# Optimization experiments

Hardware: AMD Instinct MI355X
Metric: run time of the kernel (lower is better)

The kernel has to match this reference:

```python
import jax, jax.numpy as jnp
import numpy as np

B, A, T, D, H, NB, OUT = 64, 128, 6, 256, 512, 5, 401
ALPHA = 0.5
BETA = 0.5


def _lin_init(key, n_in, n_out, extra=()):
    bound = 1.0 / np.sqrt(n_in)
    kw, kb = jax.random.split(key)
    W = jax.random.uniform(kw, extra + (n_in, n_out), minval=-bound, maxval=bound, dtype=jnp.float32)
    b = jax.random.uniform(kb, extra + (n_out,), minval=-bound, maxval=bound, dtype=jnp.float32)
    return W, b


def setup_inputs() -> dict:
    key = jax.random.key(0)
    ks = jax.random.split(key, 8)
    stdv = 1.0 / np.sqrt(D)
    anchor = jax.random.uniform(ks[0], (1, 1, T, D), minval=-stdv, maxval=stdv, dtype=jnp.float32)
    sW1, sb1 = _lin_init(ks[1], D, D, (NB,))
    sW2, sb2 = _lin_init(ks[2], D, D, (NB,))
    cW1, cb1 = _lin_init(ks[3], D, D, (NB,))
    cW2, cb2 = _lin_init(ks[4], D, D, (NB,))
    dW1, db1 = _lin_init(ks[5], D, H)
    dW2, db2 = _lin_init(ks[6], H, OUT)
    final_embedding = jax.random.normal(ks[7], (B, A, D), dtype=jnp.float32)
    return {"final_embedding": final_embedding, "anchor": anchor,
            "sW1": sW1, "sb1": sb1, "sW2": sW2, "sb2": sb2,
            "cW1": cW1, "cb1": cb1, "cW2": cW2, "cb2": cb2,
            "dW1": dW1, "db1": db1, "dW2": dW2, "db2": db2}


def _mlp2(x, W1, b1, W2, b2):
    # 2-layer MLP (Linear -> ReLU -> Linear), applied to last dim
    return jax.nn.relu(x @ W1 + b1) @ W2 + b2


def reference(final_embedding, anchor, sW1, sb1, sW2, sb2, cW1, cb1, cW2, cb2, dW1, db1, dW2, db2):
    b, a = final_embedding.shape[:2]
    # s: [B, A, T, D] repeated anchors; c: [B, A, 1, D] context
    s = jnp.broadcast_to(anchor, (b, a, T, D))
    c = final_embedding[:, :, None, :]
    for i in range(NB):
        s_new = _mlp2(s, sW1[i], sb1[i], sW2[i], sb2[i])
        c_new = _mlp2(c, cW1[i], cb1[i], cW2[i], cb2[i])
        s_new = s_new * c_new                      # gate, broadcasts over T
        agg_c = jnp.max(s_new, axis=-2, keepdims=True)
        s = ALPHA * s + BETA * s_new               # sliding running mean
        c = ALPHA * c + BETA * agg_c
    # decoder MLP on trajectory embeddings s: [B, A, T, D]
    res = jax.nn.relu(s @ dW1 + db1) @ dW2 + db2   # [B, A, T, 401]
    coordinates = res[..., :160].reshape(b, a, T, 80, 2)
    av = res[..., 160:240].reshape(b, a, T, 80, 1)
    bv = res[..., 240:320].reshape(b, a, T, 80, 1)
    cv = res[..., 320:400].reshape(b, a, T, 80, 1)
    probas = res[..., -1]                          # [B, A, T]
    cov = jnp.concatenate([jnp.exp(av) * jnp.cosh(bv), jnp.sinh(bv),
                           jnp.sinh(bv), jnp.exp(-av) * jnp.cosh(bv)], axis=-1) * jnp.exp(cv)
    covariance_matrices = cov.reshape(b, a, T, 80, 2, 2)
    return (probas, coordinates, covariance_matrices)
```

## Files before the change

kernel.cpp:

```cpp
#include <hip/hip_runtime.h>
#include <math.h>


constexpr int Tn  = 6;
constexpr int Dn  = 256;
constexpr int Hn  = 512;
constexpr int NBn = 5;
constexpr int OUTn = 401;
constexpr int BA  = 8192;
constexpr int MR  = 49152;
constexpr float kAlpha = 0.5f;
constexpr float kBeta  = 0.5f;

typedef __bf16 bf16_8 __attribute__((ext_vector_type(8)));
typedef float  f32x4  __attribute__((ext_vector_type(4)));

__device__ __forceinline__ void async_copy16(const __bf16* g, __bf16* l) {
  __builtin_amdgcn_global_load_lds(
      (const __attribute__((address_space(1))) void*)g,
      (__attribute__((address_space(3))) void*)l, 16, 0, 0);
}

template<bool RELU, bool OUT_BF16>
__global__ __launch_bounds__(256) void gemm_mfma(
    const __bf16* __restrict__ A, const __bf16* __restrict__ BT,
    const float* __restrict__ bias, void* __restrict__ Cout,
    int M, int N, int K)
{
  __shared__ __align__(16) char smem[34816];

  const int tid = threadIdx.x;
  const int l   = tid & 63;
  const int w   = tid >> 6;
  const int wm  = w >> 1, wn = w & 1;

  const int GX = gridDim.x;
  const int total = GX * gridDim.y;
  const int L = blockIdx.y * GX + blockIdx.x;
  const int xcd = L & 7, pos = L >> 3;
  const int base = total >> 3, rem = total & 7;
  const int start = xcd * base + (xcd < rem ? xcd : rem);
  const int TL = start + pos;
  const int my = TL / GX;
  const int nx = TL - my * GX;
  const int m0 = my * 128;
  const int n0 = nx * 128;

  const int lrow = l >> 2;
  const int lk   = (l & 3) * 8;
  int ar0 = m0 + w * 32 + lrow;        if (ar0 > M - 1) ar0 = M - 1;
  int ar1 = m0 + w * 32 + 16 + lrow;   if (ar1 > M - 1) ar1 = M - 1;
  int br0 = n0 + w * 32 + lrow;        if (br0 > N - 1) br0 = N - 1;
  int br1 = n0 + w * 32 + 16 + lrow;   if (br1 > N - 1) br1 = N - 1;
  const __bf16* Ag0 = A  + (size_t)ar0 * K + lk;
  const __bf16* Ag1 = A  + (size_t)ar1 * K + lk;
  const __bf16* Bg0 = BT + (size_t)br0 * K + lk;
  const __bf16* Bg1 = BT + (size_t)br1 * K + lk;

  f32x4 acc[4][4];
#pragma unroll
  for (int i = 0; i < 4; ++i)
#pragma unroll
    for (int j = 0; j < 4; ++j) acc[i][j] = (f32x4){0.f, 0.f, 0.f, 0.f};

  auto stage = [&](int buf, int ko) {
    __bf16* As = (__bf16*)(smem + buf * 16384);
    __bf16* Bs = As + 4096;
    async_copy16(Ag0 + ko, As + w * 1024);
    async_copy16(Ag1 + ko, As + w * 1024 + 512);
    async_copy16(Bg0 + ko, Bs + w * 1024);
    async_copy16(Bg1 + ko, Bs + w * 1024 + 512);
  };

  const int kIters = K >> 5;
  stage(0, 0);
  __syncthreads();
  for (int kt = 0; kt < kIters; ++kt) {
    if (kt + 1 < kIters) stage((kt + 1) & 1, (kt + 1) * 32);
    const __bf16* As = (const __bf16*)(smem + (kt & 1) * 16384);
    const __bf16* Bs = As + 4096;
    const __bf16* ap = As + (wm * 64 + (l & 15)) * 32 + (l >> 4) * 8;
    const __bf16* bp = Bs + (wn * 64 + (l & 15)) * 32 + (l >> 4) * 8;

    bf16_8 af[4], bf[4];
#pragma unroll
    for (int i = 0; i < 4; ++i) af[i] = *(const bf16_8*)(ap + i * 16 * 32);
#pragma unroll
    for (int j = 0; j < 4; ++j) bf[j] = *(const bf16_8*)(bp + j * 16 * 32);
#pragma unroll
    for (int i = 0; i < 4; ++i)
#pragma unroll
      for (int j = 0; j < 4; ++j)
        acc[i][j] = __builtin_amdgcn_mfma_f32_16x16x32_bf16(af[i], bf[j], acc[i][j], 0, 0, 0);
    __syncthreads();
  }

  const int colb = n0 + wn * 64 + (l & 15);
  const int rowb = m0 + wm * 64 + (l >> 4) * 4;

  if (OUT_BF16) {
    __bf16* Cs = (__bf16*)smem;
    const int lrb = wm * 64 + (l >> 4) * 4;
    const int lcb = wn * 64 + (l & 15);
#pragma unroll
    for (int j = 0; j < 4; ++j) {
      const float bj = bias[colb + j * 16];
#pragma unroll
      for (int i = 0; i < 4; ++i) {
#pragma unroll
        for (int r = 0; r < 4; ++r) {
          float v = acc[i][j][r] + bj;
          if (RELU) v = fmaxf(v, 0.0f);
          Cs[(lrb + i * 16 + r) * 136 + lcb + j * 16] = (__bf16)v;
        }
      }
    }
    __syncthreads();
    __bf16* Cg = (__bf16*)Cout;
#pragma unroll
    for (int it = 0; it < 8; ++it) {
      const int idx = it * 256 + tid;
      const int row = idx >> 4, c16 = idx & 15;
      const int gr = m0 + row;
      if (gr < M) {
        uint4 v = *(const uint4*)(Cs + row * 136 + c16 * 8);
        *(uint4*)(Cg + (size_t)gr * N + n0 + c16 * 8) = v;
      }
    }
  } else {
#pragma unroll
    for (int j = 0; j < 4; ++j) {
      const int gc = colb + j * 16;
      if (gc >= N) continue;
      const float bj = bias[gc];
#pragma unroll
      for (int i = 0; i < 4; ++i) {
        const int gr0 = rowb + i * 16;
#pragma unroll
        for (int r = 0; r < 4; ++r) {
          const int gr = gr0 + r;
          if (gr >= M) continue;
          float v = acc[i][j][r] + bj;
          if (RELU) v = fmaxf(v, 0.0f);
          ((float*)Cout)[(size_t)gr * N + gc] = v;
        }
      }
    }
  }
}

__global__ __launch_bounds__(512) void mlp2_c(
    const __bf16* __restrict__ X, const __bf16* __restrict__ W1T,
    const float* __restrict__ b1, const __bf16* __restrict__ W2T,
    const float* __restrict__ b2, __bf16* __restrict__ Out)
{
  __shared__ __align__(16) char smem[53248];
  __bf16* Hb = (__bf16*)(smem + 36864);

  const int tid = threadIdx.x, l = tid & 63, w = tid >> 6;
  const int m0 = blockIdx.x * 32;
  const int q4 = (l >> 4) * 4;

  f32x4 acc[2][2];
#pragma unroll
  for (int i = 0; i < 2; ++i)
#pragma unroll
    for (int j = 0; j < 2; ++j) acc[i][j] = (f32x4){0.f, 0.f, 0.f, 0.f};

  const __bf16* Xg = X + (size_t)(m0 + (tid >> 2)) * Dn + (tid & 3) * 8;

  auto stageA = [&](int buf, int kt) {
    if (tid < 128)
      async_copy16(Xg + kt * 32, (__bf16*)(smem + buf * 2048) + tid * 8);
  };
  auto stageW = [&](const __bf16* WT, int buf, int kt) {
    __bf16* Wstb = (__bf16*)(smem + 4096 + buf * 16384);
#pragma unroll
    for (int r2 = 0; r2 < 2; ++r2) {
      const int ch = tid + r2 * 512, row = ch >> 2, kk = (ch & 3) * 8;
      async_copy16(WT + (size_t)row * Dn + kt * 32 + kk, Wstb + ch * 8);
    }
  };

  stageA(0, 0); stageW(W1T, 0, 0);
  __syncthreads();
  for (int kt = 0; kt < 8; ++kt) {
    if (kt < 7) { stageA((kt + 1) & 1, kt + 1); stageW(W1T, (kt + 1) & 1, kt + 1); }
    const __bf16* Astb = (const __bf16*)(smem + (kt & 1) * 2048);
    const __bf16* Wstb = (const __bf16*)(smem + 4096 + (kt & 1) * 16384);
    bf16_8 bf[2];
#pragma unroll
    for (int j = 0; j < 2; ++j)
      bf[j] = *(const bf16_8*)(Wstb + (w * 32 + j * 16 + (l & 15)) * 32 + (l >> 4) * 8);
#pragma unroll
    for (int i = 0; i < 2; ++i) {
      bf16_8 af = *(const bf16_8*)(Astb + (i * 16 + (l & 15)) * 32 + (l >> 4) * 8);
#pragma unroll
      for (int j = 0; j < 2; ++j)
        acc[i][j] = __builtin_amdgcn_mfma_f32_16x16x32_bf16(af, bf[j], acc[i][j], 0, 0, 0);
    }
    __syncthreads();
  }

#pragma unroll
  for (int j = 0; j < 2; ++j) {
    const int col = w * 32 + j * 16 + (l & 15);
    const float bj = b1[col];
    __bf16* hc = Hb + (col >> 5) * 1024 + (col & 31);
#pragma unroll
    for (int i = 0; i < 2; ++i)
#pragma unroll
      for (int r = 0; r < 4; ++r) {
        const int row = i * 16 + q4 + r;
        hc[row * 32] = (__bf16)fmaxf(acc[i][j][r] + bj, 0.0f);
      }
  }
  __syncthreads();

#pragma unroll
  for (int i = 0; i < 2; ++i)
#pragma unroll
    for (int j = 0; j < 2; ++j) acc[i][j] = (f32x4){0.f, 0.f, 0.f, 0.f};
  stageW(W2T, 0, 0);
  __syncthreads();
  for (int kt = 0; kt < 8; ++kt) {
    if (kt < 7) stageW(W2T, (kt + 1) & 1, kt + 1);
    const __bf16* Wstb = (const __bf16*)(smem + 4096 + (kt & 1) * 16384);
    bf16_8 bf[2];
#pragma unroll
    for (int j = 0; j < 2; ++j)
      bf[j] = *(const bf16_8*)(Wstb + (w * 32 + j * 16 + (l & 15)) * 32 + (l >> 4) * 8);
#pragma unroll
    for (int i = 0; i < 2; ++i) {
      bf16_8 af = *(const bf16_8*)(Hb + kt * 1024 + (i * 16 + (l & 15)) * 32 + (l >> 4) * 8);
#pragma unroll
      for (int j = 0; j < 2; ++j)
        acc[i][j] = __builtin_amdgcn_mfma_f32_16x16x32_bf16(af, bf[j], acc[i][j], 0, 0, 0);
    }
    __syncthreads();
  }

#pragma unroll
  for (int j = 0; j < 2; ++j) {
    const int col = w * 32 + j * 16 + (l & 15);
    const float bj = b2[col];
#pragma unroll
    for (int i = 0; i < 2; ++i)
#pragma unroll
      for (int r = 0; r < 4; ++r) {
        const int row = i * 16 + q4 + r;
        Out[(size_t)(m0 + row) * Dn + col] = (__bf16)(acc[i][j][r] + bj);
      }
  }
}

__global__ __launch_bounds__(512) void mlp2_cs(
    __bf16* __restrict__ S,
    const __bf16* __restrict__ sW1T, const float* __restrict__ sb1,
    const __bf16* __restrict__ sW2T, const float* __restrict__ sb2,
    const __bf16* __restrict__ cW1T, const float* __restrict__ cb1,
    const __bf16* __restrict__ cW2T, const float* __restrict__ cb2,
    __bf16* __restrict__ C)
{
  __shared__ __align__(16) char smem[71680];
  __bf16* Hb    = (__bf16*)(smem + 22528);
  __bf16* Snew  = (__bf16*)smem;
  __bf16* Hc    = (__bf16*)(smem + 45056);
  __bf16* CnewL = (__bf16*)(smem + 53248);

  const int tid = threadIdx.x, l = tid & 63, w = tid >> 6;
  const int m0  = blockIdx.x * 96;
  const int ba0 = blockIdx.x * 16;
  const int q4  = (l >> 4) * 4;

  {
    f32x4 ac[2];
    ac[0] = (f32x4){0.f, 0.f, 0.f, 0.f};
    ac[1] = (f32x4){0.f, 0.f, 0.f, 0.f};

    const __bf16* Cg = C + (size_t)(ba0 + (tid >> 2)) * Dn + (tid & 3) * 8;

    auto stageC1 = [&](int buf, int kt) {
      __bf16* Astb = (__bf16*)(smem + buf * 22528);
      __bf16* Wstb = Astb + 3072;
      if (tid < 64) async_copy16(Cg + kt * 32, Astb + tid * 8);
#pragma unroll
      for (int r2 = 0; r2 < 2; ++r2) {
        const int ch = tid + r2 * 512, row = ch >> 2, kk = (ch & 3) * 8;
        async_copy16(cW1T + (size_t)row * Dn + kt * 32 + kk, Wstb + ch * 8);
      }
    };
    stageC1(0, 0);
    __syncthreads();
    for (int kt = 0; kt < 8; ++kt) {
      if (kt < 7) stageC1((kt + 1) & 1, kt + 1);
      const __bf16* Astb = (const __bf16*)(smem + (kt & 1) * 22528);
      const __bf16* Wstb = Astb + 3072;
      bf16_8 bf[2];
#pragma unroll
      for (int j = 0; j < 2; ++j)
        bf[j] = *(const bf16_8*)(Wstb + (w * 32 + j * 16 + (l & 15)) * 32 + (l >> 4) * 8);
      bf16_8 af = *(const bf16_8*)(Astb + (l & 15) * 32 + (l >> 4) * 8);
#pragma unroll
      for (int j = 0; j < 2; ++j)
        ac[j] = __builtin_amdgcn_mfma_f32_16x16x32_bf16(af, bf[j], ac[j], 0, 0, 0);
      __syncthreads();
    }

#pragma unroll
    for (int j = 0; j < 2; ++j) {
      const int col = w * 32 + j * 16 + (l & 15);
      const float bj = cb1[col];
      __bf16* hc = Hc + (col >> 5) * 512 + (col & 31);
#pragma unroll
      for (int r = 0; r < 4; ++r)
        hc[(q4 + r) * 32] = (__bf16)fmaxf(ac[j][r] + bj, 0.0f);
    }
    __syncthreads();

    ac[0] = (f32x4){0.f, 0.f, 0.f, 0.f};
    ac[1] = (f32x4){0.f, 0.f, 0.f, 0.f};
    auto stageC2 = [&](int buf, int kt) {
      __bf16* Wstb = (__bf16*)(smem + buf * 22528 + 6144);
#pragma unroll
      for (int r2 = 0; r2 < 2; ++r2) {
        const int ch = tid + r2 * 512, row = ch >> 2, kk = (ch & 3) * 8;
        async_copy16(cW2T + (size_t)row * Dn + kt * 32 + kk, Wstb + ch * 8);
      }
    };
    stageC2(0, 0);
    __syncthreads();
    for (int kt = 0; kt < 8; ++kt) {
      if (kt < 7) stageC2((kt + 1) & 1, kt + 1);
      const __bf16* Wstb = (const __bf16*)(smem + (kt & 1) * 22528 + 6144);
      bf16_8 bf[2];
#pragma unroll
      for (int j = 0; j < 2; ++j)
        bf[j] = *(const bf16_8*)(Wstb + (w * 32 + j * 16 + (l & 15)) * 32 + (l >> 4) * 8);
      bf16_8 af = *(const bf16_8*)(Hc + kt * 512 + (l & 15) * 32 + (l >> 4) * 8);
#pragma unroll
      for (int j = 0; j < 2; ++j)
        ac[j] = __builtin_amdgcn_mfma_f32_16x16x32_bf16(af, bf[j], ac[j], 0, 0, 0);
      __syncthreads();
    }

#pragma unroll
    for (int j = 0; j < 2; ++j) {
      const int col = w * 32 + j * 16 + (l & 15);
      const float bj = cb2[col];
#pragma unroll
      for (int r = 0; r < 4; ++r)
        CnewL[(q4 + r) * 264 + col] = (__bf16)(ac[j][r] + bj);
    }
    __syncthreads();
  }

  bf16_8 cn8 = *(const bf16_8*)(CnewL + (tid >> 5) * 264 + (tid & 31) * 8);

  f32x4 acc[6][2];
#pragma unroll
  for (int i = 0; i < 6; ++i)
#pragma unroll
    for (int j = 0; j < 2; ++j) acc[i][j] = (f32x4){0.f, 0.f, 0.f, 0.f};

  const __bf16* Sg = S + (size_t)(m0 + (tid >> 2)) * Dn + (tid & 3) * 8;

  auto stageL1 = [&](int buf, int kt) {
    __bf16* Astb = (__bf16*)(smem + buf * 22528);
    __bf16* Wstb = (__bf16*)(smem + buf * 22528 + 6144);
    if (tid < 384) async_copy16(Sg + kt * 32, Astb + tid * 8);
#pragma unroll
    for (int r2 = 0; r2 < 2; ++r2) {
      const int ch = tid + r2 * 512, row = ch >> 2, kk = (ch & 3) * 8;
      async_copy16(sW1T + (size_t)row * Dn + kt * 32 + kk, Wstb + ch * 8);
    }
  };

  stageL1(0, 0);
  __syncthreads();
  for (int kt = 0; kt < 8; ++kt) {
    if (kt < 7) stageL1((kt + 1) & 1, kt + 1);
    const __bf16* Astb = (const __bf16*)(smem + (kt & 1) * 22528);
    const __bf16* Wstb = Astb + 3072;
    bf16_8 bf[2];
#pragma unroll
    for (int j = 0; j < 2; ++j)
      bf[j] = *(const bf16_8*)(Wstb + (w * 32 + j * 16 + (l & 15)) * 32 + (l >> 4) * 8);
#pragma unroll
    for (int i = 0; i < 6; ++i) {
      bf16_8 af = *(const bf16_8*)(Astb + (i * 16 + (l & 15)) * 32 + (l >> 4) * 8);
#pragma unroll
      for (int j = 0; j < 2; ++j)
        acc[i][j] = __builtin_amdgcn_mfma_f32_16x16x32_bf16(af, bf[j], acc[i][j], 0, 0, 0);
    }
    __syncthreads();
  }

#pragma unroll
  for (int j = 0; j < 2; ++j) {
    const int col = w * 32 + j * 16 + (l & 15);
    const float bj = sb1[col];
    __bf16* hc = Hb + (col >> 5) * (96 * 32) + (col & 31);
#pragma unroll
    for (int i = 0; i < 6; ++i)
#pragma unroll
      for (int r = 0; r < 4; ++r) {
        const int row = i * 16 + q4 + r;
        hc[row * 32] = (__bf16)fmaxf(acc[i][j][r] + bj, 0.0f);
      }
  }
  __syncthreads();

#pragma unroll
  for (int i = 0; i < 6; ++i)
#pragma unroll
    for (int j = 0; j < 2; ++j) acc[i][j] = (f32x4){0.f, 0.f, 0.f, 0.f};
  __bf16* Wst = (__bf16*)(smem + 6144);
  for (int kt = 0; kt < 8; ++kt) {
#pragma unroll
    for (int r2 = 0; r2 < 2; ++r2) {
      const int ch = tid + r2 * 512, row = ch >> 2, kk = (ch & 3) * 8;
      async_copy16(sW2T + (size_t)row * Dn + kt * 32 + kk, Wst + ch * 8);
    }
    __syncthreads();
    bf16_8 bf[2];
#pragma unroll
    for (int j = 0; j < 2; ++j)
      bf[j] = *(const bf16_8*)(Wst + (w * 32 + j * 16 + (l & 15)) * 32 + (l >> 4) * 8);
#pragma unroll
    for (int i = 0; i < 6; ++i) {
      bf16_8 af = *(const bf16_8*)(Hb + kt * (96 * 32) + (i * 16 + (l & 15)) * 32 + (l >> 4) * 8);
#pragma unroll
      for (int j = 0; j < 2; ++j)
        acc[i][j] = __builtin_amdgcn_mfma_f32_16x16x32_bf16(af, bf[j], acc[i][j], 0, 0, 0);
    }
    __syncthreads();
  }

#pragma unroll
  for (int j = 0; j < 2; ++j) {
    const int col = w * 32 + j * 16 + (l & 15);
    const float bj = sb2[col];
#pragma unroll
    for (int i = 0; i < 6; ++i)
#pragma unroll
      for (int r = 0; r < 4; ++r) {
        const int row = i * 16 + q4 + r;
        Snew[row * 264 + col] = (__bf16)(acc[i][j][r] + bj);
      }
  }
  __syncthreads();

  {
    const int ba = tid >> 5, dg = (tid & 31) * 8;
    const size_t gb = (size_t)(ba0 + ba) * Dn + dg;
    float cn[8], m[8];
#pragma unroll
    for (int e = 0; e < 8; ++e) { cn[e] = (float)cn8[e]; m[e] = -3.402823466e38f; }
#pragma unroll
    for (int t = 0; t < Tn; ++t) {
      const int row = ba * 6 + t;
      bf16_8 sn8 = *(const bf16_8*)(Snew + row * 264 + dg);
      const size_t gs = (size_t)(m0 + row) * Dn + dg;
      bf16_8 s8 = *(const bf16_8*)(S + gs);
      bf16_8 o8;
#pragma unroll
      for (int e = 0; e < 8; ++e) {
        const float sn = (float)sn8[e] * cn[e];
        m[e] = fmaxf(m[e], sn);
        o8[e] = (__bf16)(kAlpha * (float)s8[e] + kBeta * sn);
      }
      *(bf16_8*)(S + gs) = o8;
    }
    bf16_8 c8 = *(const bf16_8*)(C + gb);
#pragma unroll
    for (int e = 0; e < 8; ++e)
      c8[e] = (__bf16)(kAlpha * (float)c8[e] + kBeta * m[e]);
    *(bf16_8*)(C + gb) = c8;
  }
}

__global__ __launch_bounds__(512, 4) void decoder2_fused(
    const __bf16* __restrict__ A, const __bf16* __restrict__ BT,
    const float* __restrict__ bias, float* __restrict__ out)
{
  __shared__ __align__(16) char smem[73728];
  float* mid = (float*)smem;

  const int tid = threadIdx.x, l = tid & 63, w = tid >> 6;
  const int m0 = blockIdx.x * 64;
  const int q4 = (l >> 4) * 4;

  f32x4 acc[4][4];
#pragma unroll
  for (int i = 0; i < 4; ++i)
#pragma unroll
    for (int j = 0; j < 4; ++j) acc[i][j] = (f32x4){0.f, 0.f, 0.f, 0.f};

  const __bf16* Ag = A + (size_t)(m0 + (tid >> 2)) * Hn + (tid & 3) * 8;
  const __bf16* Bg[4];
#pragma unroll
  for (int r4 = 0; r4 < 4; ++r4) {
    const int ch = tid + r4 * 512;
    int row = ch >> 2; if (row > 400) row = 400;
    Bg[r4] = BT + (size_t)row * Hn + (ch & 3) * 8;
  }

  auto stage = [&](int buf, int kt) {
    const int ko = kt * 32;
    __bf16* base = (__bf16*)(smem + buf * 36864);
    if (tid < 256) async_copy16(Ag + ko, base + tid * 8);
    __bf16* Bl = base + 64 * 32;
#pragma unroll
    for (int r4 = 0; r4 < 4; ++r4)
      async_copy16(Bg[r4] + ko, Bl + (size_t)(tid + r4 * 512) * 8);
  };

  stage(0, 0);
  __syncthreads();
  int cur = 0;
  for (int kt = 0; kt < 16; ++kt) {
    if (kt < 15) stage(cur ^ 1, kt + 1);
    const __bf16* Asl = (const __bf16*)(smem + cur * 36864);
    const __bf16* Bsl = Asl + 64 * 32;
    bf16_8 af[4], bf[4];
#pragma unroll
    for (int j = 0; j < 4; ++j)
      bf[j] = *(const bf16_8*)(Bsl + (w * 64 + j * 16 + (l & 15)) * 32 + (l >> 4) * 8);
#pragma unroll
    for (int i = 0; i < 4; ++i)
      af[i] = *(const bf16_8*)(Asl + (i * 16 + (l & 15)) * 32 + (l >> 4) * 8);
#pragma unroll
    for (int i = 0; i < 4; ++i)
#pragma unroll
      for (int j = 0; j < 4; ++j)
        acc[i][j] = __builtin_amdgcn_mfma_f32_16x16x32_bf16(af[i], bf[j], acc[i][j], 0, 0, 0);
    __syncthreads();
    cur ^= 1;
  }

  float* cov = out + MR + (size_t)MR * 160;
  const int gc = w * 64 + (l & 15);
#pragma unroll
  for (int sub = 0; sub < 2; ++sub) {
#pragma unroll
    for (int ih = 0; ih < 2; ++ih) {
      const int i = sub * 2 + ih;
#pragma unroll
      for (int j = 0; j < 4; ++j) {
        const int c = gc + j * 16;
        if (c > 400) continue;
        const float bj = bias[c];
#pragma unroll
        for (int r = 0; r < 4; ++r) {
          const int lr = ih * 16 + q4 + r;
          const int gr = m0 + sub * 32 + lr;
          const float v = acc[i][j][r] + bj;
          if (c < 160)      out[(size_t)MR + (size_t)gr * 160 + c] = v;
          else if (c < 400) mid[lr * 241 + (c - 160)] = v;
          else              out[gr] = v;
        }
      }
    }
    __syncthreads();
#pragma unroll
    for (int p = 0; p < 5; ++p) {
      const int q = p * 512 + tid;
      const int r32 = q / 80, j = q - r32 * 80;
      const int gr = m0 + sub * 32 + r32;
      const float av = mid[r32 * 241 + j];
      const float bv = mid[r32 * 241 + 80 + j];
      const float cv = mid[r32 * 241 + 160 + j];
      const float eb = __expf(bv), ebn = __expf(-bv);
      const float sh = 0.5f * (eb - ebn), ch = 0.5f * (eb + ebn);
      const float ea = __expf(av), ean = __expf(-av), ec = __expf(cv);
      f32x4 c4 = { ea * ch * ec, sh * ec, sh * ec, ean * ch * ec };
      *(f32x4*)(cov + (size_t)gr * 320 + 4 * j) = c4;
    }
    if (sub == 0) __syncthreads();
  }
}

__global__ __launch_bounds__(256) void transpose_bf16(
    const float* __restrict__ W, __bf16* __restrict__ WT, int K, int N)
{
  __shared__ float t[32][33];
  const int b  = blockIdx.z;
  const int tx = threadIdx.x, ty = threadIdx.y;
  const int k0 = blockIdx.y * 32, n0 = blockIdx.x * 32;
  const float* Wb  = W  + (size_t)b * K * N;
  __bf16*      WTb = WT + (size_t)b * N * K;
#pragma unroll
  for (int r = 0; r < 4; ++r) {
    int kk = k0 + ty + r * 8;
    if (kk < K && n0 + tx < N) t[ty + r * 8][tx] = Wb[(size_t)kk * N + n0 + tx];
  }
  __syncthreads();
#pragma unroll
  for (int r = 0; r < 4; ++r) {
    int nn = n0 + ty + r * 8;
    if (nn < N && k0 + tx < K)
      WTb[(size_t)nn * K + k0 + tx] = (__bf16)t[tx][ty + r * 8];
  }
}

__global__ __launch_bounds__(256) void convert_bf16(
    const float* __restrict__ in, __bf16* __restrict__ out, int n)
{
  int i = blockIdx.x * 256 + threadIdx.x;
  if (i < n) out[i] = (__bf16)in[i];
}

__global__ __launch_bounds__(256) void ew_update0(
    const float* __restrict__ anchor, const float* __restrict__ fe,
    const float* __restrict__ snewsm, const __bf16* __restrict__ cnew,
    __bf16* __restrict__ s, __bf16* __restrict__ c)
{
  int q = blockIdx.x * 256 + threadIdx.x;
  if (q >= BA * 32) return;
  int ba = q >> 5;
  int dg = (q & 31) * 8;
  bf16_8 cn8 = *(const bf16_8*)(cnew + (size_t)ba * Dn + dg);
  float cn[8], m[8];
#pragma unroll
  for (int e = 0; e < 8; ++e) { cn[e] = (float)cn8[e]; m[e] = -3.402823466e38f; }
  size_t base = (size_t)ba * Tn * Dn + dg;
#pragma unroll
  for (int t = 0; t < Tn; ++t) {
    bf16_8 o8;
#pragma unroll
    for (int e = 0; e < 8; ++e) {
      float sn = snewsm[t * Dn + dg + e] * cn[e];
      m[e] = fmaxf(m[e], sn);
      o8[e] = (__bf16)(kAlpha * anchor[t * Dn + dg + e] + kBeta * sn);
    }
    *(bf16_8*)(s + base + t * Dn) = o8;
  }
  bf16_8 c8;
#pragma unroll
  for (int e = 0; e < 8; ++e)
    c8[e] = (__bf16)(kAlpha * fe[(size_t)ba * Dn + dg + e] + kBeta * m[e]);
  *(bf16_8*)(c + (size_t)ba * Dn + dg) = c8;
}

extern "C" void kernel_launch(void* const* d_in, const int* in_sizes, int n_in,
                              void* d_out, int out_size, void* d_ws, size_t ws_size,
                              hipStream_t stream) {
  const float* fe     = (const float*)d_in[0];
  const float* anchor = (const float*)d_in[1];
  const float* sW1 = (const float*)d_in[2];
  const float* sb1 = (const float*)d_in[3];
  const float* sW2 = (const float*)d_in[4];
  const float* sb2 = (const float*)d_in[5];
  const float* cW1 = (const float*)d_in[6];
  const float* cb1 = (const float*)d_in[7];
  const float* cW2 = (const float*)d_in[8];
  const float* cb2 = (const float*)d_in[9];
  const float* dW1 = (const float*)d_in[10];
  const float* db1 = (const float*)d_in[11];
  const float* dW2 = (const float*)d_in[12];
  const float* db2 = (const float*)d_in[13];
  float* out = (float*)d_out;

  char* p = (char*)d_ws;
  __bf16* s_bf    = (__bf16*)(p + 0);
  __bf16* hd_bf   = (__bf16*)(p + 25165824);
  __bf16* c_bf    = (__bf16*)(p + 75497472);
  __bf16* cnew_bf = (__bf16*)(p + 79691776);
  __bf16* fe_bf   = (__bf16*)(p + 83886080);
  __bf16* sWT1    = (__bf16*)(p + 88080384);
  __bf16* sWT2    = (__bf16*)(p + 88735744);
  __bf16* cWT1    = (__bf16*)(p + 89391104);
  __bf16* cWT2    = (__bf16*)(p + 90046464);
  __bf16* dWT1    = (__bf16*)(p + 90701824);
  __bf16* dWT2    = (__bf16*)(p + 90963968);
  __bf16* anc_bf  = (__bf16*)(p + 91374592);
  __bf16* hsm_bf  = (__bf16*)(p + 91377664);
  float*  snewsm_f= (float* )(p + 91380736);

  auto gemm = [&](const __bf16* A, const __bf16* BT, const float* b, void* C,
                  int M, int N, int K, bool relu, bool outbf) {
    dim3 grid((N + 127) / 128, (M + 127) / 128);
    if (relu) {
      if (outbf) gemm_mfma<true,  true ><<<grid, 256, 0, stream>>>(A, BT, b, C, M, N, K);
      else       gemm_mfma<true,  false><<<grid, 256, 0, stream>>>(A, BT, b, C, M, N, K);
    } else {
      if (outbf) gemm_mfma<false, true ><<<grid, 256, 0, stream>>>(A, BT, b, C, M, N, K);
      else       gemm_mfma<false, false><<<grid, 256, 0, stream>>>(A, BT, b, C, M, N, K);
    }
  };

  {
    dim3 blk(32, 8);
    dim3 g88(8, 8, NBn);
    transpose_bf16<<<g88, blk, 0, stream>>>(sW1, sWT1, Dn, Dn);
    transpose_bf16<<<g88, blk, 0, stream>>>(sW2, sWT2, Dn, Dn);
    transpose_bf16<<<g88, blk, 0, stream>>>(cW1, cWT1, Dn, Dn);
    transpose_bf16<<<g88, blk, 0, stream>>>(cW2, cWT2, Dn, Dn);
    transpose_bf16<<<dim3(16, 8, 1), blk, 0, stream>>>(dW1, dWT1, Dn, Hn);
    transpose_bf16<<<dim3(13, 16, 1), blk, 0, stream>>>(dW2, dWT2, Hn, OUTn);
  }
  convert_bf16<<<(BA * Dn + 255) / 256, 256, 0, stream>>>(fe, fe_bf, BA * Dn);
  convert_bf16<<<(Tn * Dn + 255) / 256, 256, 0, stream>>>(anchor, anc_bf, Tn * Dn);

  const size_t WKK = (size_t)Dn * Dn;

  gemm(anc_bf, sWT1, sb1, hsm_bf,   Tn, Dn, Dn, true,  true);
  gemm(hsm_bf, sWT2, sb2, snewsm_f, Tn, Dn, Dn, false, false);
  mlp2_c<<<BA / 32, 512, 0, stream>>>(fe_bf, cWT1, cb1, cWT2, cb2, cnew_bf);
  ew_update0<<<(BA * 32 + 255) / 256, 256, 0, stream>>>(anchor, fe, snewsm_f,
                                                        cnew_bf, s_bf, c_bf);

  for (int i = 1; i < NBn; ++i) {
    mlp2_cs<<<MR / 96, 512, 0, stream>>>(
        s_bf,
        sWT1 + i * WKK, sb1 + i * Dn, sWT2 + i * WKK, sb2 + i * Dn,
        cWT1 + i * WKK, cb1 + i * Dn, cWT2 + i * WKK, cb2 + i * Dn,
        c_bf);
  }

  gemm(s_bf, dWT1, db1, hd_bf, MR, Hn, Dn, true, true);
  decoder2_fused<<<MR / 64, 512, 0, stream>>>(hd_bf, dWT2, db2, out);
}
```

Before: 374.4 us.

## Fuse decoder first-layer GEMM into second-layer kernel via LDS hidden chunks

The decoder's first linear+ReLU is now computed inside the second-layer kernel in 64-column chunks. Each chunk's hidden activations live in shared memory and are consumed immediately by the output GEMM. This removes writing and re-reading the large bf16 hidden buffer in global memory and drops one kernel launch. In exchange, the first GEMM runs with tight per-step synchronisation and partial-thread loads, W2 fragments are read directly from global memory per chunk, and occupancy hints change.

After: 662.4 us. 1.77x slower.

```diff
diff --git a/kernel.cpp b/kernel.cpp
--- a/kernel.cpp
+++ b/kernel.cpp
@@ -480,16 +480,22 @@
   }
 }
 
-__global__ __launch_bounds__(512, 4) void decoder2_fused(
-    const __bf16* __restrict__ A, const __bf16* __restrict__ BT,
+__global__ __launch_bounds__(512, 6) void decoder_fused(
+    const __bf16* __restrict__ S, const __bf16* __restrict__ W1T,
+    const float* __restrict__ b1, const __bf16* __restrict__ W2T,
     const float* __restrict__ bias, float* __restrict__ out)
 {
-  __shared__ __align__(16) char smem[73728];
-  float* mid = (float*)smem;
+  __shared__ __align__(16) char smem[49152];
+  __bf16* Ast = (__bf16*)smem;
+  __bf16* W1s = (__bf16*)(smem + 32768);
+  __bf16* Hb  = (__bf16*)(smem + 40960);
+  float*  mid = (float*)smem;
 
   const int tid = threadIdx.x, l = tid & 63, w = tid >> 6;
   const int m0 = blockIdx.x * 64;
   const int q4 = (l >> 4) * 4;
+  const int rt  = w >> 1;
+  const int ch2 = (w & 1) * 32;
 
   f32x4 acc[4][4];
 #pragma unroll
@@ -497,46 +503,72 @@
 #pragma unroll
     for (int j = 0; j < 4; ++j) acc[i][j] = (f32x4){0.f, 0.f, 0.f, 0.f};
 
-  const __bf16* Ag = A + (size_t)(m0 + (tid >> 2)) * Hn + (tid & 3) * 8;
-  const __bf16* Bg[4];
-#pragma unroll
-  for (int r4 = 0; r4 < 4; ++r4) {
-    const int ch = tid + r4 * 512;
-    int row = ch >> 2; if (row > 400) row = 400;
-    Bg[r4] = BT + (size_t)row * Hn + (ch & 3) * 8;
-  }
-
-  auto stage = [&](int buf, int kt) {
-    const int ko = kt * 32;
-    __bf16* base = (__bf16*)(smem + buf * 36864);
-    if (tid < 256) async_copy16(Ag + ko, base + tid * 8);
-    __bf16* Bl = base + 64 * 32;
-#pragma unroll
-    for (int r4 = 0; r4 < 4; ++r4)
-      async_copy16(Bg[r4] + ko, Bl + (size_t)(tid + r4 * 512) * 8);
-  };
-
-  stage(0, 0);
-  __syncthreads();
-  int cur = 0;
-  for (int kt = 0; kt < 16; ++kt) {
-    if (kt < 15) stage(cur ^ 1, kt + 1);
-    const __bf16* Asl = (const __bf16*)(smem + cur * 36864);
-    const __bf16* Bsl = Asl + 64 * 32;
-    bf16_8 af[4], bf[4];
-#pragma unroll
-    for (int j = 0; j < 4; ++j)
-      bf[j] = *(const bf16_8*)(Bsl + (w * 64 + j * 16 + (l & 15)) * 32 + (l >> 4) * 8);
-#pragma unroll
-    for (int i = 0; i < 4; ++i)
-      af[i] = *(const bf16_8*)(Asl + (i * 16 + (l & 15)) * 32 + (l >> 4) * 8);
-#pragma unroll
-    for (int i = 0; i < 4; ++i)
-#pragma unroll
-      for (int j = 0; j < 4; ++j)
-        acc[i][j] = __builtin_amdgcn_mfma_f32_16x16x32_bf16(af[i], bf[j], acc[i][j], 0, 0, 0);
-    __syncthreads();
-    cur ^= 1;
+  if (tid < 256) {
+    const __bf16* Sg = S + (size_t)(m0 + (tid >> 2)) * Dn + (tid & 3) * 8;
+#pragma unroll
+    for (int kt = 0; kt < 8; ++kt)
+      async_copy16(Sg + kt * 32, Ast + kt * 2048 + tid * 8);
+  }
+
+  const int wkk = (tid & 3) * 8;
+
+  for (int cc = 0; cc < 8; ++cc) {
+    if (tid < 256)
+      async_copy16(W1T + (size_t)(cc * 64 + (tid >> 2)) * Dn + wkk,
+                   W1s + tid * 8);
+
+    bf16_8 bf2[2][4];
+#pragma unroll
+    for (int j = 0; j < 4; ++j) {
+      int col = w * 64 + j * 16 + (l & 15);
+      if (col > 400) col = 400;
+      const __bf16* bp = W2T + (size_t)col * Hn + cc * 64 + (l >> 4) * 8;
+      bf2[0][j] = *(const bf16_8*)(bp);
+      bf2[1][j] = *(const bf16_8*)(bp + 32);
+    }
+    __syncthreads();
+
+    f32x4 a1[2];
+    a1[0] = (f32x4){0.f, 0.f, 0.f, 0.f};
+    a1[1] = (f32x4){0.f, 0.f, 0.f, 0.f};
+    for (int kt = 0; kt < 8; ++kt) {
+      if (kt < 7 && tid < 256)
+        async_copy16(W1T + (size_t)(cc * 64 + (tid >> 2)) * Dn + (kt + 1) * 32 + wkk,
+                     W1s + ((kt + 1) & 1) * 2048 + tid * 8);
+      const __bf16* Wb = W1s + (kt & 1) * 2048;
+      bf16_8 af = *(const bf16_8*)(Ast + kt * 2048 + (rt * 16 + (l & 15)) * 32 + (l >> 4) * 8);
+#pragma unroll
+      for (int j = 0; j < 2; ++j) {
+        bf16_8 bw = *(const bf16_8*)(Wb + (ch2 + j * 16 + (l & 15)) * 32 + (l >> 4) * 8);
+        a1[j] = __builtin_amdgcn_mfma_f32_16x16x32_bf16(af, bw, a1[j], 0, 0, 0);
+      }
+      __syncthreads();
+    }
+
+#pragma unroll
+    for (int j = 0; j < 2; ++j) {
+      const int col = ch2 + j * 16 + (l & 15);
+      const float bj = b1[cc * 64 + col];
+      __bf16* hp = Hb + (col >> 5) * 2048 + (col & 31);
+#pragma unroll
+      for (int r = 0; r < 4; ++r)
+        hp[(rt * 16 + q4 + r) * 32] = (__bf16)fmaxf(a1[j][r] + bj, 0.0f);
+    }
+    __syncthreads();
+
+#pragma unroll
+    for (int kt2 = 0; kt2 < 2; ++kt2) {
+      bf16_8 af2[4];
+#pragma unroll
+      for (int i = 0; i < 4; ++i)
+        af2[i] = *(const bf16_8*)(Hb + kt2 * 2048 + (i * 16 + (l & 15)) * 32 + (l >> 4) * 8);
+#pragma unroll
+      for (int i = 0; i < 4; ++i)
+#pragma unroll
+        for (int j = 0; j < 4; ++j)
+          acc[i][j] = __builtin_amdgcn_mfma_f32_16x16x32_bf16(af2[i], bf2[kt2][j], acc[i][j], 0, 0, 0);
+    }
+    __syncthreads();
   }
 
   float* cov = out + MR + (size_t)MR * 160;
@@ -664,7 +696,6 @@
 
   char* p = (char*)d_ws;
   __bf16* s_bf    = (__bf16*)(p + 0);
-  __bf16* hd_bf   = (__bf16*)(p + 25165824);
   __bf16* c_bf    = (__bf16*)(p + 75497472);
   __bf16* cnew_bf = (__bf16*)(p + 79691776);
   __bf16* fe_bf   = (__bf16*)(p + 83886080);
@@ -719,6 +750,5 @@
         c_bf);
   }
 
-  gemm(s_bf, dWT1, db1, hd_bf, MR, Hn, Dn, true, true);
-  decoder2_fused<<<MR / 64, 512, 0, stream>>>(hd_bf, dWT2, db2, out);
-}
+  decoder_fused<<<MR / 64, 512, 0, stream>>>(s_bf, dWT1, db1, dWT2, db2, out);
+}
```
